# Kernel tuning notes

Measured on AMD Instinct MI355X. Metric: run time of the kernel, lower is better.

The kernel has to match this reference:

```python
import jax, jax.numpy as jnp
import numpy as np


def _ln(x, g, eps=1e-5):
    # channel LayerNorm over dim 1, unbiased=False variance
    mean = jnp.mean(x, axis=1, keepdims=True)
    var = jnp.mean((x - mean) ** 2, axis=1, keepdims=True)
    return (x - mean) * jax.lax.rsqrt(var + eps) * g


def _c11(x, w, b):
    # 1x1 conv: w (O,C), b (O,)
    return jnp.einsum('bchw,oc->bohw', x, w) + b[None, :, None, None]


def _dw(x, w, b):
    # depthwise 3x3 conv, SAME padding; w (C,1,3,3), b (C,)
    C = x.shape[1]
    y = jax.lax.conv_general_dilated(x, w, (1, 1), 'SAME',
                                     feature_group_count=C,
                                     dimension_numbers=('NCHW', 'OIHW', 'NCHW'))
    return y + b[None, :, None, None]


def _forward(F_i, F_w, g1, g2, qw1, qb1, kw1, kb1, vw1, vb1,
             qw2, qb2, kw2, kb2, vw2, vb2,
             qdw1, qdb1, kdw1, kdb1, vdw1, vdb1,
             qdw2, qdb2, kdw2, kdb2, vdw2, vdb2, lw, lb):
    B, C1, H, W = F_i.shape
    C2 = F_w.shape[1]
    HW = H * W
    fi = _ln(F_i, g1)
    fw = _ln(F_w, g2)
    # qkv = 1x1 conv -> depthwise conv; then RAW C-order reshape (torch .view)
    Qi = _dw(_c11(fi, qw1, qb1), qdw1, qdb1).reshape(B, HW, C1)
    Ki = _dw(_c11(fi, kw1, kb1), kdw1, kdb1).reshape(B, HW, C1)
    Vi = _dw(_c11(fi, vw1, vb1), vdw1, vdb1).reshape(B, C1, HW)
    Qw = _dw(_c11(fw, qw2, qb2), qdw2, qdb2).reshape(B, HW, C2)
    Kw = _dw(_c11(fw, kw2, kb2), kdw2, kdb2).reshape(B, HW, C2)
    Vw = _dw(_c11(fw, vw2, vb2), vdw2, vdb2).reshape(B, C2, HW)
    # channel cross-attention: (B,C1,HW)@(B,HW,C2) -> (B,C1,C2)
    a1 = jax.nn.softmax(jnp.einsum('bnc,bnd->bcd', Qi, Kw), axis=-1)
    a2 = jax.nn.softmax(jnp.einsum('bnc,bnd->bcd', Qw, Ki), axis=-1)
    Aw = jnp.einsum('bcd,bdn->bcn', a1, Vw).reshape(B, H, W, C2).transpose(0, 3, 1, 2)
    Ai = jnp.einsum('bcd,bdn->bcn', a2, Vi).reshape(B, H, W, C1).transpose(0, 3, 1, 2)
    cat = jnp.concatenate([Aw, Ai], axis=1)  # (B, C2+C1, H, W)
    Ct = cat.shape[1]
    flat = cat.reshape(B, Ct, HW).transpose(0, 2, 1).reshape(-1, Ct)  # (B*HW, Ct)
    out = flat @ lw.T + lb  # (B*HW, Cout)
    Cout = lb.shape[0]
    # faithful replication of torch's view/permute/view tail
    out = out.reshape(B, Cout, H, W).transpose(0, 2, 3, 1).reshape(B, Cout, H, W)
    return out + F_i + F_w


def setup_inputs() -> dict:
    key = jax.random.key(0)
    ks = jax.random.split(key, 20)
    B, C, H, W = 8, 128, 128, 128
    d = {}
    d['F_i'] = jax.random.normal(ks[0], (B, C, H, W), jnp.float32)
    d['F_w'] = jax.random.normal(ks[1], (B, C, H, W), jnp.float32)
    d['g1'] = jnp.ones((1, C, 1, 1), jnp.float32)
    d['g2'] = jnp.ones((1, C, 1, 1), jnp.float32)
    s = 1.0 / np.sqrt(C)
    i = 2
    for n in ['qw1', 'kw1', 'vw1', 'qw2', 'kw2', 'vw2']:
        d[n] = jax.random.normal(ks[i], (C, C), jnp.float32) * s
        i += 1
    for n in ['qb1', 'kb1', 'vb1', 'qb2', 'kb2', 'vb2']:
        d[n] = jnp.zeros((C,), jnp.float32)
    sd = 1.0 / 3.0
    for n in ['qdw1', 'kdw1', 'vdw1', 'qdw2', 'kdw2', 'vdw2']:
        d[n] = jax.random.normal(ks[i], (C, 1, 3, 3), jnp.float32) * sd
        i += 1
    for n in ['qdb1', 'kdb1', 'vdb1', 'qdb2', 'kdb2', 'vdb2']:
        d[n] = jnp.zeros((C,), jnp.float32)
    d['lw'] = jax.random.normal(ks[i], (C, 2 * C), jnp.float32) * (1.0 / np.sqrt(2 * C))
    d['lb'] = jnp.zeros((C,), jnp.float32)
    return d


def reference(F_i, F_w, g1, g2, qw1, qb1, kw1, kb1, vw1, vb1,
              qw2, qb2, kw2, kb2, vw2, vb2,
              qdw1, qdb1, kdw1, kdb1, vdw1, vdb1,
              qdw2, qdb2, kdw2, kdb2, vdw2, vdb2, lw, lb):
    return _forward(F_i, F_w, g1, g2, qw1, qb1, kw1, kb1, vw1, vb1,
                    qw2, qb2, kw2, kb2, vw2, vb2,
                    qdw1, qdb1, kdw1, kdb1, vdw1, vdb1,
                    qdw2, qdb2, kdw2, kdb2, vdw2, vdb2, lw, lb)
```

## Files before the change

### kernel.cpp

```cpp
#include <hip/hip_runtime.h>
#include <cstddef>
#include <cstring>

#define HW 16384
#define CC 128
#define NB 8
#define GB 4

typedef short bf16x8_t __attribute__((ext_vector_type(8)));
typedef float floatx4 __attribute__((ext_vector_type(4)));

__device__ inline unsigned short f2bf(float f) {
  unsigned u; __builtin_memcpy(&u, &f, 4);
  u += 0x7fffu + ((u >> 16) & 1u);
  return (unsigned short)(u >> 16);
}
__device__ inline float bf2f(unsigned short s) {
  unsigned u = ((unsigned)s) << 16; float f; __builtin_memcpy(&f, &u, 4);
  return f;
}

__global__ __launch_bounds__(256) void k_ln_stats(const float* __restrict__ x,
                                                  float* __restrict__ mean,
                                                  float* __restrict__ rstd) {
  int idx = blockIdx.x * 256 + threadIdx.x;
  int b = idx >> 14;
  int p = idx & (HW - 1);
  const float* xp = x + ((size_t)b << 21) + p;
  float s = 0.f, ss = 0.f;
  for (int c = 0; c < CC; ++c) {
    float v = xp[(size_t)c << 14];
    s += v;
    ss += v * v;
  }
  float m = s * (1.0f / CC);
  float var = ss * (1.0f / CC) - m * m;
  mean[idx] = m;
  rstd[idx] = rsqrtf(var + 1e-5f);
}

__global__ __launch_bounds__(256) void k_conv1x1_mfma(
    const float* __restrict__ X, const float* __restrict__ W,
    const float* __restrict__ bias, const float* __restrict__ g,
    const float* __restrict__ mean, const float* __restrict__ rstd,
    float* __restrict__ Y, int b0) {
  __shared__ __align__(16) float raw[32][132];
  __shared__ __align__(16) short Ah[128][40];
  __shared__ __align__(16) short Al[128][40];
  __shared__ __align__(16) short Bh[128][40];
  __shared__ __align__(16) short Bl[128][40];
  const int bl = blockIdx.y;
  const int b = b0 + bl;
  const int p0 = blockIdx.x * 128;
  const int t = threadIdx.x;
  const int lane = t & 63, wv = t >> 6;
  const int quad = lane >> 4, l15 = lane & 15;
  const int wr = wv >> 1, wc = wv & 1;

  const int s1c = t >> 3, s1p = (t & 7) * 16;
  const int sao = t >> 1, sas = (t & 1) * 16;
  const int s2p = t & 127, s2o = t >> 7;
  const float mu = mean[b * HW + p0 + s2p];
  const float rs = rstd[b * HW + p0 + s2p];

  const float* Xb = X + ((size_t)b << 21);
  floatx4 acc[4][4];
#pragma unroll
  for (int i = 0; i < 4; ++i)
#pragma unroll
    for (int j = 0; j < 4; ++j) acc[i][j] = (floatx4){0.f, 0.f, 0.f, 0.f};

  for (int k0 = 0; k0 < 128; k0 += 32) {
    {
      const float* xp = Xb + ((size_t)(k0 + s1c) << 14) + p0 + s1p;
#pragma unroll
      for (int u = 0; u < 4; ++u)
        *reinterpret_cast<float4*>(&raw[s1c][s1p + 4 * u]) =
            *reinterpret_cast<const float4*>(xp + 4 * u);
    }
    {
      const float* wp = W + sao * 128 + k0 + sas;
      const float* gp = g + k0 + sas;
      short th[16], tl[16];
#pragma unroll
      for (int j = 0; j < 16; ++j) {
        float v = wp[j] * gp[j];
        unsigned short h = f2bf(v);
        th[j] = (short)h;
        tl[j] = (short)f2bf(v - bf2f(h));
      }
#pragma unroll
      for (int j = 0; j < 2; ++j) {
        *reinterpret_cast<bf16x8_t*>(&Ah[sao][sas + 8 * j]) =
            *reinterpret_cast<bf16x8_t*>(&th[8 * j]);
        *reinterpret_cast<bf16x8_t*>(&Al[sao][sas + 8 * j]) =
            *reinterpret_cast<bf16x8_t*>(&tl[8 * j]);
      }
    }
    __syncthreads();
#pragma unroll
    for (int item = 0; item < 2; ++item) {
      const int oct = s2o + 2 * item;
      short th[8], tl[8];
#pragma unroll
      for (int jj = 0; jj < 8; ++jj) {
        float v = (raw[oct * 8 + jj][s2p] - mu) * rs;
        unsigned short h = f2bf(v);
        th[jj] = (short)h;
        tl[jj] = (short)f2bf(v - bf2f(h));
      }
      *reinterpret_cast<bf16x8_t*>(&Bh[s2p][oct * 8]) =
          *reinterpret_cast<bf16x8_t*>(&th[0]);
      *reinterpret_cast<bf16x8_t*>(&Bl[s2p][oct * 8]) =
          *reinterpret_cast<bf16x8_t*>(&tl[0]);
    }
    __syncthreads();
    bf16x8_t afh[4], afl[4], bfh[4], bfl[4];
#pragma unroll
    for (int i = 0; i < 4; ++i) {
      const int m = wr * 64 + i * 16 + l15;
      afh[i] = *reinterpret_cast<const bf16x8_t*>(&Ah[m][quad * 8]);
      afl[i] = *reinterpret_cast<const bf16x8_t*>(&Al[m][quad * 8]);
    }
#pragma unroll
    for (int j = 0; j < 4; ++j) {
      const int p = wc * 64 + j * 16 + l15;
      bfh[j] = *reinterpret_cast<const bf16x8_t*>(&Bh[p][quad * 8]);
      bfl[j] = *reinterpret_cast<const bf16x8_t*>(&Bl[p][quad * 8]);
    }
#pragma unroll
    for (int i = 0; i < 4; ++i)
#pragma unroll
      for (int j = 0; j < 4; ++j) {
        acc[i][j] = __builtin_amdgcn_mfma_f32_16x16x32_bf16(afh[i], bfh[j], acc[i][j], 0, 0, 0);
        acc[i][j] = __builtin_amdgcn_mfma_f32_16x16x32_bf16(afh[i], bfl[j], acc[i][j], 0, 0, 0);
        acc[i][j] = __builtin_amdgcn_mfma_f32_16x16x32_bf16(afl[i], bfh[j], acc[i][j], 0, 0, 0);
      }
    __syncthreads();
  }
  float* Yb = Y + ((size_t)bl << 21);
#pragma unroll
  for (int i = 0; i < 4; ++i) {
#pragma unroll
    for (int j = 0; j < 4; ++j) {
#pragma unroll
      for (int r = 0; r < 4; ++r) {
        const int o = wr * 64 + i * 16 + quad * 4 + r;
        const int p = p0 + wc * 64 + j * 16 + l15;
        Yb[((size_t)o << 14) + p] = acc[i][j][r] + bias[o];
      }
    }
  }
}

__global__ __launch_bounds__(256) void k_score_mfma(
    const float* __restrict__ Yq, const float* __restrict__ Yk,
    const float* __restrict__ qdw, const float* __restrict__ qdb,
    const float* __restrict__ kdw, const float* __restrict__ kdb,
    float* __restrict__ P) {
  __shared__ __align__(16) float raw[32][132];
  __shared__ __align__(16) short Ah[128][40];
  __shared__ __align__(16) short Al[128][40];
  __shared__ __align__(16) short Bh[128][40];
  __shared__ __align__(16) short Bl[128][40];
  const int ch = blockIdx.x;
  const int bl = blockIdx.y;
  const int t = threadIdx.x;
  const int lane = t & 63, wv = t >> 6;
  const int quad = lane >> 4, l15 = lane & 15;
  const int wr = wv >> 1, wc = wv & 1;
  const int h_loc = t >> 3;
  const int w0 = (t & 7) * 16;
  const int s2w = t & 127, s2o = t >> 7;
  const int cc = ch;
  const float* Yqb = Yq + ((size_t)bl << 21) + ((size_t)cc << 14);
  const float* Ykb = Yk + ((size_t)bl << 21) + ((size_t)cc << 14);
  const float* qwt = qdw + cc * 9;
  const float* kwt = kdw + cc * 9;
  const float qbv = qdb[cc], kbv = kdb[cc];

  floatx4 acc[4][4];
#pragma unroll
  for (int i = 0; i < 4; ++i)
#pragma unroll
    for (int j = 0; j < 4; ++j) acc[i][j] = (floatx4){0.f, 0.f, 0.f, 0.f};

  for (int k0 = 0; k0 < 128; k0 += 32) {
    const int h = k0 + h_loc;
#pragma unroll
    for (int side = 0; side < 2; ++side) {
      const float* Yc = side ? Ykb : Yqb;
      const float* wt = side ? kwt : qwt;
      const float bias = side ? kbv : qbv;
      float a[16];
#pragma unroll
      for (int j = 0; j < 16; ++j) a[j] = bias;
#pragma unroll
      for (int dy = 0; dy < 3; ++dy) {
        const int hh = h + dy - 1;
        if (hh < 0 || hh > 127) continue;
        const float* rp = Yc + (hh << 7) + w0;
        float4 f0 = *reinterpret_cast<const float4*>(rp);
        float4 f1 = *reinterpret_cast<const float4*>(rp + 4);
        float4 f2 = *reinterpret_cast<const float4*>(rp + 8);
        float4 f3 = *reinterpret_cast<const float4*>(rp + 12);
        float s[18];
        s[1] = f0.x;  s[2] = f0.y;  s[3] = f0.z;  s[4] = f0.w;
        s[5] = f1.x;  s[6] = f1.y;  s[7] = f1.z;  s[8] = f1.w;
        s[9] = f2.x;  s[10] = f2.y; s[11] = f2.z; s[12] = f2.w;
        s[13] = f3.x; s[14] = f3.y; s[15] = f3.z; s[16] = f3.w;
        s[0] = (w0 > 0) ? rp[-1] : 0.f;
        s[17] = (w0 < 112) ? rp[16] : 0.f;
        const float wa = wt[dy * 3 + 0], wb = wt[dy * 3 + 1], wc2 = wt[dy * 3 + 2];
#pragma unroll
        for (int j = 0; j < 16; ++j)
          a[j] = fmaf(s[j], wa, fmaf(s[j + 1], wb, fmaf(s[j + 2], wc2, a[j])));
      }
#pragma unroll
      for (int u = 0; u < 4; ++u)
        *reinterpret_cast<float4*>(&raw[h_loc][w0 + 4 * u]) =
            (float4){a[4 * u], a[4 * u + 1], a[4 * u + 2], a[4 * u + 3]};
      __syncthreads();
      short* dh = side ? &Bh[0][0] : &Ah[0][0];
      short* dl = side ? &Bl[0][0] : &Al[0][0];
#pragma unroll
      for (int item = 0; item < 2; ++item) {
        const int oct = s2o + 2 * item;
        short th[8], tl[8];
#pragma unroll
        for (int jj = 0; jj < 8; ++jj) {
          float v = raw[oct * 8 + jj][s2w];
          unsigned short hb = f2bf(v);
          th[jj] = (short)hb;
          tl[jj] = (short)f2bf(v - bf2f(hb));
        }
        *reinterpret_cast<bf16x8_t*>(&dh[s2w * 40 + oct * 8]) =
            *reinterpret_cast<bf16x8_t*>(&th[0]);
        *reinterpret_cast<bf16x8_t*>(&dl[s2w * 40 + oct * 8]) =
            *reinterpret_cast<bf16x8_t*>(&tl[0]);
      }
      __syncthreads();
    }
    bf16x8_t afh[4], afl[4], bfh[4], bfl[4];
#pragma unroll
    for (int i = 0; i < 4; ++i) {
      const int m = wr * 64 + i * 16 + l15;
      afh[i] = *reinterpret_cast<const bf16x8_t*>(&Ah[m][quad * 8]);
      afl[i] = *reinterpret_cast<const bf16x8_t*>(&Al[m][quad * 8]);
    }
#pragma unroll
    for (int j = 0; j < 4; ++j) {
      const int n = wc * 64 + j * 16 + l15;
      bfh[j] = *reinterpret_cast<const bf16x8_t*>(&Bh[n][quad * 8]);
      bfl[j] = *reinterpret_cast<const bf16x8_t*>(&Bl[n][quad * 8]);
    }
#pragma unroll
    for (int i = 0; i < 4; ++i)
#pragma unroll
      for (int j = 0; j < 4; ++j) {
        acc[i][j] = __builtin_amdgcn_mfma_f32_16x16x32_bf16(afh[i], bfh[j], acc[i][j], 0, 0, 0);
        acc[i][j] = __builtin_amdgcn_mfma_f32_16x16x32_bf16(afh[i], bfl[j], acc[i][j], 0, 0, 0);
        acc[i][j] = __builtin_amdgcn_mfma_f32_16x16x32_bf16(afl[i], bfh[j], acc[i][j], 0, 0, 0);
      }
  }
  float* Pp = P + ((size_t)(ch * GB + bl) << 14);
#pragma unroll
  for (int i = 0; i < 4; ++i) {
#pragma unroll
    for (int j = 0; j < 4; ++j) {
#pragma unroll
      for (int r = 0; r < 4; ++r) {
        const int c = wr * 64 + i * 16 + quad * 4 + r;
        const int d = wc * 64 + j * 16 + l15;
        Pp[c * 128 + d] = acc[i][j][r];
      }
    }
  }
}

__global__ __launch_bounds__(256) void k_score_reduce(const float* __restrict__ P,
                                                      float* __restrict__ S) {
  int idx = blockIdx.x * 256 + threadIdx.x;
  int bl = idx >> 14;
  int rem = idx & 16383;
  float s = 0.f;
  for (int c = 0; c < 128; ++c) s += P[((size_t)(c * GB + bl) << 14) + rem];
  S[idx] = s;
}

__global__ __launch_bounds__(128) void k_softmax(float* __restrict__ S) {
  __shared__ float red[128];
  const int row = blockIdx.x;
  const int t = threadIdx.x;
  float v = S[row * 128 + t];
  red[t] = v;
  __syncthreads();
  for (int s = 64; s > 0; s >>= 1) {
    if (t < s) red[t] = fmaxf(red[t], red[t + s]);
    __syncthreads();
  }
  float mx = red[0];
  __syncthreads();
  float e = expf(v - mx);
  red[t] = e;
  __syncthreads();
  for (int s = 64; s > 0; s >>= 1) {
    if (t < s) red[t] += red[t + s];
    __syncthreads();
  }
  S[row * 128 + t] = e / red[0];
}

__global__ __launch_bounds__(256) void k_dw_t(const float* __restrict__ Y,
                                              const float* __restrict__ Kw,
                                              const float* __restrict__ db,
                                              unsigned short* __restrict__ Vt) {
  __shared__ unsigned short T[128][33];
  const int h = blockIdx.x;
  const int c0 = blockIdx.y * 32;
  const int bl = blockIdx.z;
  const int t = threadIdx.x;
  const int cl = t >> 3;
  const int w0 = (t & 7) * 16;
  const int c = c0 + cl;
  const float* Yc = Y + ((size_t)bl << 21) + ((size_t)c << 14);
  const float* wt = Kw + c * 9;
  float a[16];
#pragma unroll
  for (int j = 0; j < 16; ++j) a[j] = db[c];
#pragma unroll
  for (int dy = 0; dy < 3; ++dy) {
    const int hh = h + dy - 1;
    if (hh < 0 || hh > 127) continue;
    const float* rp = Yc + (hh << 7) + w0;
    float4 f0 = *reinterpret_cast<const float4*>(rp);
    float4 f1 = *reinterpret_cast<const float4*>(rp + 4);
    float4 f2 = *reinterpret_cast<const float4*>(rp + 8);
    float4 f3 = *reinterpret_cast<const float4*>(rp + 12);
    float s[18];
    s[1] = f0.x;  s[2] = f0.y;  s[3] = f0.z;  s[4] = f0.w;
    s[5] = f1.x;  s[6] = f1.y;  s[7] = f1.z;  s[8] = f1.w;
    s[9] = f2.x;  s[10] = f2.y; s[11] = f2.z; s[12] = f2.w;
    s[13] = f3.x; s[14] = f3.y; s[15] = f3.z; s[16] = f3.w;
    s[0] = (w0 > 0) ? rp[-1] : 0.f;
    s[17] = (w0 < 112) ? rp[16] : 0.f;
    const float wa = wt[dy * 3 + 0], wb = wt[dy * 3 + 1], wc2 = wt[dy * 3 + 2];
#pragma unroll
    for (int j = 0; j < 16; ++j)
      a[j] = fmaf(s[j], wa, fmaf(s[j + 1], wb, fmaf(s[j + 2], wc2, a[j])));
  }
#pragma unroll
  for (int j = 0; j < 16; ++j) T[w0 + j][cl] = f2bf(a[j]);
  __syncthreads();
  const int w = t >> 1, half = t & 1;
  unsigned short tmp[16];
#pragma unroll
  for (int j = 0; j < 16; ++j) tmp[j] = T[w][half * 16 + j];
  uint4 v0, v1;
  unsigned* vp0 = reinterpret_cast<unsigned*>(&v0);
  unsigned* vp1 = reinterpret_cast<unsigned*>(&v1);
#pragma unroll
  for (int j = 0; j < 4; ++j) {
    vp0[j] = (unsigned)tmp[2 * j] | ((unsigned)tmp[2 * j + 1] << 16);
    vp1[j] = (unsigned)tmp[8 + 2 * j] | ((unsigned)tmp[8 + 2 * j + 1] << 16);
  }
  unsigned short* dst = Vt + ((size_t)bl << 21) + ((size_t)((h << 7) + w) << 7)
                        + c0 + half * 16;
  *reinterpret_cast<uint4*>(dst) = v0;
  *reinterpret_cast<uint4*>(dst + 8) = v1;
}

__global__ __launch_bounds__(256) void k_av_mfma(
    const float* __restrict__ S, const unsigned short* __restrict__ Vt,
    unsigned short* __restrict__ O) {
  __shared__ __align__(16) short As[128][136];
  const int bl = blockIdx.y;
  const int p0 = blockIdx.x * 128;
  const int t = threadIdx.x;
  const int lane = t & 63, wv = t >> 6;
  const int quad = lane >> 4, l15 = lane & 15;
  const int wr = wv >> 1, wc = wv & 1;
  {
    const float* Ab = S + ((size_t)bl << 14);
    const int r = t >> 1, hf = (t & 1) * 64;
    const float* src = Ab + r * 128 + hf;
    short tmp[64];
#pragma unroll
    for (int j = 0; j < 64; ++j) tmp[j] = (short)f2bf(src[j]);
#pragma unroll
    for (int j = 0; j < 8; ++j)
      *reinterpret_cast<bf16x8_t*>(&As[r][hf + j * 8]) =
          *reinterpret_cast<bf16x8_t*>(&tmp[j * 8]);
  }
  __syncthreads();
  floatx4 acc[4][4];
#pragma unroll
  for (int i = 0; i < 4; ++i)
#pragma unroll
    for (int j = 0; j < 4; ++j) acc[i][j] = (floatx4){0.f, 0.f, 0.f, 0.f};
  const unsigned short* Vb = Vt + ((size_t)bl << 21);
#pragma unroll
  for (int d0 = 0; d0 < 128; d0 += 32) {
    bf16x8_t af[4], bf[4];
#pragma unroll
    for (int i = 0; i < 4; ++i) {
      const int m = wr * 64 + i * 16 + l15;
      af[i] = *reinterpret_cast<const bf16x8_t*>(&As[m][d0 + quad * 8]);
    }
#pragma unroll
    for (int j = 0; j < 4; ++j) {
      const int p = p0 + wc * 64 + j * 16 + l15;
      bf[j] = *reinterpret_cast<const bf16x8_t*>(Vb + ((size_t)p << 7) + d0 + quad * 8);
    }
#pragma unroll
    for (int i = 0; i < 4; ++i)
#pragma unroll
      for (int j = 0; j < 4; ++j)
        acc[i][j] = __builtin_amdgcn_mfma_f32_16x16x32_bf16(af[i], bf[j], acc[i][j], 0, 0, 0);
  }
  unsigned short* Ob = O + ((size_t)bl << 21);
#pragma unroll
  for (int i = 0; i < 4; ++i) {
#pragma unroll
    for (int j = 0; j < 4; ++j) {
#pragma unroll
      for (int r = 0; r < 4; ++r) {
        const int c = wr * 64 + i * 16 + quad * 4 + r;
        const int p = p0 + wc * 64 + j * 16 + l15;
        Ob[((size_t)c << 14) + p] = f2bf(acc[i][j][r]);
      }
    }
  }
}

__global__ __launch_bounds__(256) void k_final2_mfma(
    const unsigned short* __restrict__ A1, const unsigned short* __restrict__ A2,
    const float* __restrict__ lw, const float* __restrict__ lb,
    const float* __restrict__ Fi, const float* __restrict__ Fw,
    float* __restrict__ out, int b0) {
  __shared__ __align__(16) short As[128][136];
  const int c2 = blockIdx.x;
  const int bl = blockIdx.y;
  const int b = b0 + bl;
  const int t = threadIdx.x;
  const int lane = t & 63, wv = t >> 6;
  const int quad = lane >> 4, l15 = lane & 15;
  const int wr = wv >> 1, wc = wv & 1;
  floatx4 acc[4][4];
#pragma unroll
  for (int i = 0; i < 4; ++i)
#pragma unroll
    for (int j = 0; j < 4; ++j) acc[i][j] = (floatx4){0.f, 0.f, 0.f, 0.f};
#pragma unroll
  for (int phase = 0; phase < 2; ++phase) {
    {
      const int r = t >> 1, hf = (t & 1) * 64;
      const float* src = lw + r * 256 + phase * 128 + hf;
      short tmp[64];
#pragma unroll
      for (int j = 0; j < 64; ++j) tmp[j] = (short)f2bf(src[j]);
#pragma unroll
      for (int j = 0; j < 8; ++j)
        *reinterpret_cast<bf16x8_t*>(&As[r][hf + j * 8]) =
            *reinterpret_cast<bf16x8_t*>(&tmp[j * 8]);
    }
    __syncthreads();
    const unsigned short* Ub = (phase ? A2 : A1) + ((size_t)bl << 21) + c2 * 128;
#pragma unroll
    for (int d0 = 0; d0 < 128; d0 += 32) {
      bf16x8_t af[4], bf[4];
#pragma unroll
      for (int i = 0; i < 4; ++i) {
        const int m = wr * 64 + i * 16 + l15;
        af[i] = *reinterpret_cast<const bf16x8_t*>(&As[m][d0 + quad * 8]);
      }
#pragma unroll
      for (int j = 0; j < 4; ++j) {
        const int n = wc * 64 + j * 16 + l15;
        bf[j] = *reinterpret_cast<const bf16x8_t*>(Ub + ((size_t)n << 14) + d0 + quad * 8);
      }
#pragma unroll
      for (int i = 0; i < 4; ++i)
#pragma unroll
        for (int j = 0; j < 4; ++j)
          acc[i][j] = __builtin_amdgcn_mfma_f32_16x16x32_bf16(af[i], bf[j], acc[i][j], 0, 0, 0);
    }
    __syncthreads();
  }
  const size_t obase = ((size_t)b << 21) + ((size_t)c2 << 14);
#pragma unroll
  for (int i = 0; i < 4; ++i) {
#pragma unroll
    for (int j = 0; j < 4; ++j) {
#pragma unroll
      for (int r = 0; r < 4; ++r) {
        const int h2 = wr * 64 + i * 16 + quad * 4 + r;
        const int w2 = wc * 64 + j * 16 + l15;
        const size_t a = obase + ((size_t)h2 << 7) + w2;
        out[a] = acc[i][j][r] + lb[h2] + Fi[a] + Fw[a];
      }
    }
  }
}

extern "C" void kernel_launch(void* const* d_in, const int* in_sizes, int n_in,
                              void* d_out, int out_size, void* d_ws, size_t ws_size,
                              hipStream_t stream) {
  const float* F_i  = (const float*)d_in[0];
  const float* F_w  = (const float*)d_in[1];
  const float* g1   = (const float*)d_in[2];
  const float* g2   = (const float*)d_in[3];
  const float* qw1  = (const float*)d_in[4];
  const float* kw1  = (const float*)d_in[5];
  const float* vw1  = (const float*)d_in[6];
  const float* qw2  = (const float*)d_in[7];
  const float* kw2  = (const float*)d_in[8];
  const float* vw2  = (const float*)d_in[9];
  const float* qb1  = (const float*)d_in[10];
  const float* kb1  = (const float*)d_in[11];
  const float* vb1  = (const float*)d_in[12];
  const float* qb2  = (const float*)d_in[13];
  const float* kb2  = (const float*)d_in[14];
  const float* vb2  = (const float*)d_in[15];
  const float* qdw1 = (const float*)d_in[16];
  const float* kdw1 = (const float*)d_in[17];
  const float* vdw1 = (const float*)d_in[18];
  const float* qdw2 = (const float*)d_in[19];
  const float* kdw2 = (const float*)d_in[20];
  const float* vdw2 = (const float*)d_in[21];
  const float* qdb1 = (const float*)d_in[22];
  const float* kdb1 = (const float*)d_in[23];
  const float* vdb1 = (const float*)d_in[24];
  const float* qdb2 = (const float*)d_in[25];
  const float* kdb2 = (const float*)d_in[26];
  const float* vdb2 = (const float*)d_in[27];
  const float* lw   = (const float*)d_in[28];
  const float* lb   = (const float*)d_in[29];
  float* out = (float*)d_out;

  char* w = (char*)d_ws;
  const size_t NTOT = (size_t)NB * HW;
  float* meanI = (float*)w; w += NTOT * 4;
  float* rstdI = (float*)w; w += NTOT * 4;
  float* meanW = (float*)w; w += NTOT * 4;
  float* rstdW = (float*)w; w += NTOT * 4;
  float* S     = (float*)w; w += (size_t)GB * HW * 4;
  float* P     = (float*)w; w += (size_t)128 * GB * HW * 4;
  float* Yq    = (float*)w; w += ((size_t)GB << 21) * 4;
  char*  Ykreg = w;         w += ((size_t)GB << 21) * 4;
  float* Yk    = (float*)Ykreg;
  unsigned short* Vt = (unsigned short*)Ykreg;
  unsigned short* A2 = (unsigned short*)(Ykreg + ((size_t)GB << 21) * 2);
  unsigned short* A1 = (unsigned short*)w; w += ((size_t)GB << 21) * 2;

  dim3 blk(256);
  k_ln_stats<<<dim3(512), blk, 0, stream>>>(F_i, meanI, rstdI);
  k_ln_stats<<<dim3(512), blk, 0, stream>>>(F_w, meanW, rstdW);

  for (int b0 = 0; b0 < NB; b0 += GB) {
    k_conv1x1_mfma<<<dim3(128, GB), blk, 0, stream>>>(F_i, qw1, qb1, g1, meanI, rstdI, Yq, b0);
    k_conv1x1_mfma<<<dim3(128, GB), blk, 0, stream>>>(F_w, kw2, kb2, g2, meanW, rstdW, Yk, b0);
    k_score_mfma<<<dim3(128, GB), blk, 0, stream>>>(Yq, Yk, qdw1, qdb1, kdw2, kdb2, P);
    k_score_reduce<<<dim3(GB * HW / 256), blk, 0, stream>>>(P, S);
    k_softmax<<<dim3(GB * 128), dim3(128), 0, stream>>>(S);
    k_conv1x1_mfma<<<dim3(128, GB), blk, 0, stream>>>(F_w, vw2, vb2, g2, meanW, rstdW, Yq, b0);
    k_dw_t<<<dim3(128, 4, GB), blk, 0, stream>>>(Yq, vdw2, vdb2, Vt);
    k_av_mfma<<<dim3(128, GB), blk, 0, stream>>>(S, Vt, A1);

    k_conv1x1_mfma<<<dim3(128, GB), blk, 0, stream>>>(F_w, qw2, qb2, g2, meanW, rstdW, Yq, b0);
    k_conv1x1_mfma<<<dim3(128, GB), blk, 0, stream>>>(F_i, kw1, kb1, g1, meanI, rstdI, Yk, b0);
    k_score_mfma<<<dim3(128, GB), blk, 0, stream>>>(Yq, Yk, qdw2, qdb2, kdw1, kdb1, P);
    k_score_reduce<<<dim3(GB * HW / 256), blk, 0, stream>>>(P, S);
    k_softmax<<<dim3(GB * 128), dim3(128), 0, stream>>>(S);
    k_conv1x1_mfma<<<dim3(128, GB), blk, 0, stream>>>(F_i, vw1, vb1, g1, meanI, rstdI, Yq, b0);
    k_dw_t<<<dim3(128, 4, GB), blk, 0, stream>>>(Yq, vdw1, vdb1, Vt);
    k_av_mfma<<<dim3(128, GB), blk, 0, stream>>>(S, Vt, A2);

    k_final2_mfma<<<dim3(128, GB), blk, 0, stream>>>(A1, A2, lw, lb, F_i, F_w, out, b0);
  }
}
```

Before: 843.2 us.

## Fuse K/V projections and replace per-channel score partials with atomic accumulation

Adds a kernel that computes the K and V 1x1 projections together, so the normalized input tile is loaded and converted once per pass instead of twice. The score kernel no longer writes one partial matrix per channel block into a large buffer; it atomically adds into 8 partial slices. Reduction of those slices is fused into the softmax kernel, which removes the separate reduce kernel and a large write/read of partial sums. This adds a zeroing launch and atomic contention, and the workspace is re-laid out so the partial buffer aliases the A2 region.

```diff
diff --git a/kernel.cpp b/kernel.cpp
--- a/kernel.cpp
+++ b/kernel.cpp
@@ -153,11 +153,164 @@
   }
 }
 
+__global__ __launch_bounds__(256) void k_convKV_mfma(
+    const float* __restrict__ X,
+    const float* __restrict__ Wk, const float* __restrict__ kb,
+    const float* __restrict__ Wv, const float* __restrict__ vb,
+    const float* __restrict__ g,
+    const float* __restrict__ mean, const float* __restrict__ rstd,
+    float* __restrict__ Yk, float* __restrict__ Yv, int b0) {
+  __shared__ __align__(16) float raw[32][68];
+  __shared__ __align__(16) short Kh[128][40];
+  __shared__ __align__(16) short Kl[128][40];
+  __shared__ __align__(16) short Vh[128][40];
+  __shared__ __align__(16) short Vl[128][40];
+  __shared__ __align__(16) short Bh[64][40];
+  __shared__ __align__(16) short Bl[64][40];
+  const int bl = blockIdx.y;
+  const int b = b0 + bl;
+  const int p0 = blockIdx.x * 64;
+  const int t = threadIdx.x;
+  const int lane = t & 63, wv = t >> 6;
+  const int quad = lane >> 4, l15 = lane & 15;
+  const int wr = wv >> 1, wc = wv & 1;
+
+  const int s1c = t >> 3, s1p = (t & 7) * 8;
+  const int sao = t >> 1, sas = (t & 1) * 16;
+  const int s2p = t & 63, s2o = t >> 6;
+  const float mu = mean[b * HW + p0 + s2p];
+  const float rs = rstd[b * HW + p0 + s2p];
+
+  const float* Xb = X + ((size_t)b << 21);
+  floatx4 accK[4][2], accV[4][2];
+#pragma unroll
+  for (int i = 0; i < 4; ++i)
+#pragma unroll
+    for (int j = 0; j < 2; ++j) {
+      accK[i][j] = (floatx4){0.f, 0.f, 0.f, 0.f};
+      accV[i][j] = (floatx4){0.f, 0.f, 0.f, 0.f};
+    }
+
+  for (int k0 = 0; k0 < 128; k0 += 32) {
+    {
+      const float* xp = Xb + ((size_t)(k0 + s1c) << 14) + p0 + s1p;
+      *reinterpret_cast<float4*>(&raw[s1c][s1p]) =
+          *reinterpret_cast<const float4*>(xp);
+      *reinterpret_cast<float4*>(&raw[s1c][s1p + 4]) =
+          *reinterpret_cast<const float4*>(xp + 4);
+    }
+    {
+      const float* gp = g + k0 + sas;
+      const float* wkp = Wk + sao * 128 + k0 + sas;
+      const float* wvp = Wv + sao * 128 + k0 + sas;
+      short th[16], tl[16];
+#pragma unroll
+      for (int j = 0; j < 16; ++j) {
+        float v = wkp[j] * gp[j];
+        unsigned short h = f2bf(v);
+        th[j] = (short)h;
+        tl[j] = (short)f2bf(v - bf2f(h));
+      }
+#pragma unroll
+      for (int j = 0; j < 2; ++j) {
+        *reinterpret_cast<bf16x8_t*>(&Kh[sao][sas + 8 * j]) =
+            *reinterpret_cast<bf16x8_t*>(&th[8 * j]);
+        *reinterpret_cast<bf16x8_t*>(&Kl[sao][sas + 8 * j]) =
+            *reinterpret_cast<bf16x8_t*>(&tl[8 * j]);
+      }
+#pragma unroll
+      for (int j = 0; j < 16; ++j) {
+        float v = wvp[j] * gp[j];
+        unsigned short h = f2bf(v);
+        th[j] = (short)h;
+        tl[j] = (short)f2bf(v - bf2f(h));
+      }
+#pragma unroll
+      for (int j = 0; j < 2; ++j) {
+        *reinterpret_cast<bf16x8_t*>(&Vh[sao][sas + 8 * j]) =
+            *reinterpret_cast<bf16x8_t*>(&th[8 * j]);
+        *reinterpret_cast<bf16x8_t*>(&Vl[sao][sas + 8 * j]) =
+            *reinterpret_cast<bf16x8_t*>(&tl[8 * j]);
+      }
+    }
+    __syncthreads();
+    {
+      short th[8], tl[8];
+#pragma unroll
+      for (int jj = 0; jj < 8; ++jj) {
+        float v = (raw[s2o * 8 + jj][s2p] - mu) * rs;
+        unsigned short h = f2bf(v);
+        th[jj] = (short)h;
+        tl[jj] = (short)f2bf(v - bf2f(h));
+      }
+      *reinterpret_cast<bf16x8_t*>(&Bh[s2p][s2o * 8]) =
+          *reinterpret_cast<bf16x8_t*>(&th[0]);
+      *reinterpret_cast<bf16x8_t*>(&Bl[s2p][s2o * 8]) =
+          *reinterpret_cast<bf16x8_t*>(&tl[0]);
+    }
+    __syncthreads();
+    bf16x8_t bfh[2], bfl[2];
+#pragma unroll
+    for (int j = 0; j < 2; ++j) {
+      const int p = wc * 32 + j * 16 + l15;
+      bfh[j] = *reinterpret_cast<const bf16x8_t*>(&Bh[p][quad * 8]);
+      bfl[j] = *reinterpret_cast<const bf16x8_t*>(&Bl[p][quad * 8]);
+    }
+    {
+      bf16x8_t ah[4], al[4];
+#pragma unroll
+      for (int i = 0; i < 4; ++i) {
+        const int m = wr * 64 + i * 16 + l15;
+        ah[i] = *reinterpret_cast<const bf16x8_t*>(&Kh[m][quad * 8]);
+        al[i] = *reinterpret_cast<const bf16x8_t*>(&Kl[m][quad * 8]);
+      }
+#pragma unroll
+      for (int i = 0; i < 4; ++i)
+#pragma unroll
+        for (int j = 0; j < 2; ++j) {
+          accK[i][j] = __builtin_amdgcn_mfma_f32_16x16x32_bf16(ah[i], bfh[j], accK[i][j], 0, 0, 0);
+          accK[i][j] = __builtin_amdgcn_mfma_f32_16x16x32_bf16(ah[i], bfl[j], accK[i][j], 0, 0, 0);
+          accK[i][j] = __builtin_amdgcn_mfma_f32_16x16x32_bf16(al[i], bfh[j], accK[i][j], 0, 0, 0);
+        }
+#pragma unroll
+      for (int i = 0; i < 4; ++i) {
+        const int m = wr * 64 + i * 16 + l15;
+        ah[i] = *reinterpret_cast<const bf16x8_t*>(&Vh[m][quad * 8]);
+        al[i] = *reinterpret_cast<const bf16x8_t*>(&Vl[m][quad * 8]);
+      }
+#pragma unroll
+      for (int i = 0; i < 4; ++i)
+#pragma unroll
+        for (int j = 0; j < 2; ++j) {
+          accV[i][j] = __builtin_amdgcn_mfma_f32_16x16x32_bf16(ah[i], bfh[j], accV[i][j], 0, 0, 0);
+          accV[i][j] = __builtin_amdgcn_mfma_f32_16x16x32_bf16(ah[i], bfl[j], accV[i][j], 0, 0, 0);
+          accV[i][j] = __builtin_amdgcn_mfma_f32_16x16x32_bf16(al[i], bfh[j], accV[i][j], 0, 0, 0);
+        }
+    }
+    __syncthreads();
+  }
+  float* Ykb = Yk + ((size_t)bl << 21);
+  float* Yvb = Yv + ((size_t)bl << 21);
+#pragma unroll
+  for (int i = 0; i < 4; ++i) {
+#pragma unroll
+    for (int j = 0; j < 2; ++j) {
+#pragma unroll
+      for (int r = 0; r < 4; ++r) {
+        const int o = wr * 64 + i * 16 + quad * 4 + r;
+        const int p = p0 + wc * 32 + j * 16 + l15;
+        Ykb[((size_t)o << 14) + p] = accK[i][j][r] + kb[o];
+        Yvb[((size_t)o << 14) + p] = accV[i][j][r] + vb[o];
+      }
+    }
+  }
+}
+
 __global__ __launch_bounds__(256) void k_score_mfma(
     const float* __restrict__ Yq, const float* __restrict__ Yk,
     const float* __restrict__ qdw, const float* __restrict__ qdb,
     const float* __restrict__ kdw, const float* __restrict__ kdb,
-    float* __restrict__ P) {
+    float* __restrict__ P8) {
   __shared__ __align__(16) float raw[32][132];
   __shared__ __align__(16) short Ah[128][40];
   __shared__ __align__(16) short Al[128][40];
@@ -263,7 +416,7 @@
         acc[i][j] = __builtin_amdgcn_mfma_f32_16x16x32_bf16(afl[i], bfh[j], acc[i][j], 0, 0, 0);
       }
   }
-  float* Pp = P + ((size_t)(ch * GB + bl) << 14);
+  float* Pp = P8 + ((size_t)((ch & 7) * GB + bl) << 14);
 #pragma unroll
   for (int i = 0; i < 4; ++i) {
 #pragma unroll
@@ -272,27 +425,26 @@
       for (int r = 0; r < 4; ++r) {
         const int c = wr * 64 + i * 16 + quad * 4 + r;
         const int d = wc * 64 + j * 16 + l15;
-        Pp[c * 128 + d] = acc[i][j][r];
-      }
-    }
-  }
-}
-
-__global__ __launch_bounds__(256) void k_score_reduce(const float* __restrict__ P,
-                                                      float* __restrict__ S) {
-  int idx = blockIdx.x * 256 + threadIdx.x;
-  int bl = idx >> 14;
-  int rem = idx & 16383;
-  float s = 0.f;
-  for (int c = 0; c < 128; ++c) s += P[((size_t)(c * GB + bl) << 14) + rem];
-  S[idx] = s;
-}
-
-__global__ __launch_bounds__(128) void k_softmax(float* __restrict__ S) {
+        (void)__hip_atomic_fetch_add(&Pp[c * 128 + d], acc[i][j][r],
+                                     __ATOMIC_RELAXED, __HIP_MEMORY_SCOPE_AGENT);
+      }
+    }
+  }
+}
+
+__global__ __launch_bounds__(256) void k_zero(float4* __restrict__ p) {
+  p[blockIdx.x * 256 + threadIdx.x] = (float4){0.f, 0.f, 0.f, 0.f};
+}
+
+__global__ __launch_bounds__(128) void k_reduce8_softmax(
+    const float* __restrict__ P8, float* __restrict__ S) {
   __shared__ float red[128];
   const int row = blockIdx.x;
   const int t = threadIdx.x;
-  float v = S[row * 128 + t];
+  const size_t base = ((size_t)row << 7) + t;
+  float v = 0.f;
+#pragma unroll
+  for (int k = 0; k < 8; ++k) v += P8[(((size_t)(k * GB)) << 14) + base];
   red[t] = v;
   __syncthreads();
   for (int s = 64; s > 0; s >>= 1) {
@@ -308,7 +460,7 @@
     if (t < s) red[t] += red[t + s];
     __syncthreads();
   }
-  S[row * 128 + t] = e / red[0];
+  S[base] = e / red[0];
 }
 
 __global__ __launch_bounds__(256) void k_dw_t(const float* __restrict__ Y,
@@ -545,35 +697,35 @@
   float* meanW = (float*)w; w += NTOT * 4;
   float* rstdW = (float*)w; w += NTOT * 4;
   float* S     = (float*)w; w += (size_t)GB * HW * 4;
-  float* P     = (float*)w; w += (size_t)128 * GB * HW * 4;
-  float* Yq    = (float*)w; w += ((size_t)GB << 21) * 4;
-  char*  Ykreg = w;         w += ((size_t)GB << 21) * 4;
-  float* Yk    = (float*)Ykreg;
-  unsigned short* Vt = (unsigned short*)Ykreg;
-  unsigned short* A2 = (unsigned short*)(Ykreg + ((size_t)GB << 21) * 2);
   unsigned short* A1 = (unsigned short*)w; w += ((size_t)GB << 21) * 2;
+  unsigned short* A2 = (unsigned short*)w;
+  float* P8 = (float*)A2;
+  w += ((size_t)GB << 21) * 2;
+  float* Yk  = (float*)w; w += ((size_t)GB << 21) * 4;
+  float* Yqv = (float*)w; w += ((size_t)GB << 21) * 4;
+  unsigned short* Vt = (unsigned short*)w; w += ((size_t)GB << 21) * 2;
 
   dim3 blk(256);
   k_ln_stats<<<dim3(512), blk, 0, stream>>>(F_i, meanI, rstdI);
   k_ln_stats<<<dim3(512), blk, 0, stream>>>(F_w, meanW, rstdW);
 
   for (int b0 = 0; b0 < NB; b0 += GB) {
-    k_conv1x1_mfma<<<dim3(128, GB), blk, 0, stream>>>(F_i, qw1, qb1, g1, meanI, rstdI, Yq, b0);
-    k_conv1x1_mfma<<<dim3(128, GB), blk, 0, stream>>>(F_w, kw2, kb2, g2, meanW, rstdW, Yk, b0);
-    k_score_mfma<<<dim3(128, GB), blk, 0, stream>>>(Yq, Yk, qdw1, qdb1, kdw2, kdb2, P);
-    k_score_reduce<<<dim3(GB * HW / 256), blk, 0, stream>>>(P, S);
-    k_softmax<<<dim3(GB * 128), dim3(128), 0, stream>>>(S);
-    k_conv1x1_mfma<<<dim3(128, GB), blk, 0, stream>>>(F_w, vw2, vb2, g2, meanW, rstdW, Yq, b0);
-    k_dw_t<<<dim3(128, 4, GB), blk, 0, stream>>>(Yq, vdw2, vdb2, Vt);
+    k_convKV_mfma<<<dim3(256, GB), blk, 0, stream>>>(F_w, kw2, kb2, vw2, vb2,
+                                                     g2, meanW, rstdW, Yk, Yqv, b0);
+    k_dw_t<<<dim3(128, 4, GB), blk, 0, stream>>>(Yqv, vdw2, vdb2, Vt);
+    k_conv1x1_mfma<<<dim3(128, GB), blk, 0, stream>>>(F_i, qw1, qb1, g1, meanI, rstdI, Yqv, b0);
+    k_zero<<<dim3(512), blk, 0, stream>>>((float4*)P8);
+    k_score_mfma<<<dim3(128, GB), blk, 0, stream>>>(Yqv, Yk, qdw1, qdb1, kdw2, kdb2, P8);
+    k_reduce8_softmax<<<dim3(GB * 128), dim3(128), 0, stream>>>(P8, S);
     k_av_mfma<<<dim3(128, GB), blk, 0, stream>>>(S, Vt, A1);
 
-    k_conv1x1_mfma<<<dim3(128, GB), blk, 0, stream>>>(F_w, qw2, qb2, g2, meanW, rstdW, Yq, b0);
-    k_conv1x1_mfma<<<dim3(128, GB), blk, 0, stream>>>(F_i, kw1, kb1, g1, meanI, rstdI, Yk, b0);
-    k_score_mfma<<<dim3(128, GB), blk, 0, stream>>>(Yq, Yk, qdw2, qdb2, kdw1, kdb1, P);
-    k_score_reduce<<<dim3(GB * HW / 256), blk, 0, stream>>>(P, S);
-    k_softmax<<<dim3(GB * 128), dim3(128), 0, stream>>>(S);
-    k_conv1x1_mfma<<<dim3(128, GB), blk, 0, stream>>>(F_i, vw1, vb1, g1, meanI, rstdI, Yq, b0);
-    k_dw_t<<<dim3(128, 4, GB), blk, 0, stream>>>(Yq, vdw1, vdb1, Vt);
+    k_convKV_mfma<<<dim3(256, GB), blk, 0, stream>>>(F_i, kw1, kb1, vw1, vb1,
+                                                     g1, meanI, rstdI, Yk, Yqv, b0);
+    k_dw_t<<<dim3(128, 4, GB), blk, 0, stream>>>(Yqv, vdw1, vdb1, Vt);
+    k_conv1x1_mfma<<<dim3(128, GB), blk, 0, stream>>>(F_w, qw2, qb2, g2, meanW, rstdW, Yqv, b0);
+    k_zero<<<dim3(512), blk, 0, stream>>>((float4*)P8);
+    k_score_mfma<<<dim3(128, GB), blk, 0, stream>>>(Yqv, Yk, qdw2, qdb2, kdw1, kdb1, P8);
+    k_reduce8_softmax<<<dim3(GB * 128), dim3(128), 0, stream>>>(P8, S);
     k_av_mfma<<<dim3(128, GB), blk, 0, stream>>>(S, Vt, A2);
 
     k_final2_mfma<<<dim3(128, GB), blk, 0, stream>>>(A1, A2, lw, lb, F_i, F_w, out, b0);
```

Measured after the change: 927.6 us. 1.1x slower.

## Precompute split-bf16 weights once and fuse score reduce with softmax

Applied to the files above, without the earlier changes.

Adds a prep kernel that converts the six gamma-scaled 1x1 conv weights into hi/lo bf16 pairs and converts the final linear weight to bf16 once per call. The conv, AV and final kernels then read these fragments straight from global memory and no longer convert per block through shared memory. The partial-score reduction and softmax become one kernel that writes bf16 probabilities. This removes redundant conversion work, a launch and some syncs, at the cost of uncoalesced global fragment loads that depend on cache hits.

```diff
diff --git a/kernel.cpp b/kernel.cpp
--- a/kernel.cpp
+++ b/kernel.cpp
@@ -18,6 +18,39 @@
 __device__ inline float bf2f(unsigned short s) {
   unsigned u = ((unsigned)s) << 16; float f; __builtin_memcpy(&f, &u, 4);
   return f;
+}
+
+__global__ __launch_bounds__(256) void k_prep_w(
+    const float* __restrict__ qw1, const float* __restrict__ kw1,
+    const float* __restrict__ vw1, const float* __restrict__ qw2,
+    const float* __restrict__ kw2, const float* __restrict__ vw2,
+    const float* __restrict__ g1, const float* __restrict__ g2,
+    const float* __restrict__ lw,
+    unsigned short* __restrict__ Wsplit, unsigned short* __restrict__ lwbf) {
+  const int t = threadIdx.x;
+  const int m = blockIdx.y;
+  if (m < 6) {
+    const float* W = (m == 0) ? qw1 : (m == 1) ? kw1 : (m == 2) ? vw1
+                   : (m == 3) ? qw2 : (m == 4) ? kw2 : vw2;
+    const float* g = (m < 3) ? g1 : g2;
+    const int idx = blockIdx.x * 256 + t;
+    const int o = idx >> 4;
+    const int c0 = (idx & 15) * 8;
+    unsigned short* hi = Wsplit + m * 32768 + o * 128 + c0;
+    unsigned short* lo = hi + 16384;
+#pragma unroll
+    for (int j = 0; j < 8; ++j) {
+      float v = W[o * 128 + c0 + j] * g[c0 + j];
+      unsigned short h = f2bf(v);
+      hi[j] = h;
+      lo[j] = f2bf(v - bf2f(h));
+    }
+  } else {
+    const int idx = blockIdx.x * 256 + t;
+#pragma unroll
+    for (int j = 0; j < 16; ++j)
+      lwbf[idx * 16 + j] = f2bf(lw[idx * 16 + j]);
+  }
 }
 
 __global__ __launch_bounds__(256) void k_ln_stats(const float* __restrict__ x,
@@ -40,13 +73,12 @@
 }
 
 __global__ __launch_bounds__(256) void k_conv1x1_mfma(
-    const float* __restrict__ X, const float* __restrict__ W,
-    const float* __restrict__ bias, const float* __restrict__ g,
+    const float* __restrict__ X,
+    const unsigned short* __restrict__ Whi, const unsigned short* __restrict__ Wlo,
+    const float* __restrict__ bias,
     const float* __restrict__ mean, const float* __restrict__ rstd,
     float* __restrict__ Y, int b0) {
   __shared__ __align__(16) float raw[32][132];
-  __shared__ __align__(16) short Ah[128][40];
-  __shared__ __align__(16) short Al[128][40];
   __shared__ __align__(16) short Bh[128][40];
   __shared__ __align__(16) short Bl[128][40];
   const int bl = blockIdx.y;
@@ -58,7 +90,6 @@
   const int wr = wv >> 1, wc = wv & 1;
 
   const int s1c = t >> 3, s1p = (t & 7) * 16;
-  const int sao = t >> 1, sas = (t & 1) * 16;
   const int s2p = t & 127, s2o = t >> 7;
   const float mu = mean[b * HW + p0 + s2p];
   const float rs = rstd[b * HW + p0 + s2p];
@@ -77,25 +108,6 @@
       for (int u = 0; u < 4; ++u)
         *reinterpret_cast<float4*>(&raw[s1c][s1p + 4 * u]) =
             *reinterpret_cast<const float4*>(xp + 4 * u);
-    }
-    {
-      const float* wp = W + sao * 128 + k0 + sas;
-      const float* gp = g + k0 + sas;
-      short th[16], tl[16];
-#pragma unroll
-      for (int j = 0; j < 16; ++j) {
-        float v = wp[j] * gp[j];
-        unsigned short h = f2bf(v);
-        th[j] = (short)h;
-        tl[j] = (short)f2bf(v - bf2f(h));
-      }
-#pragma unroll
-      for (int j = 0; j < 2; ++j) {
-        *reinterpret_cast<bf16x8_t*>(&Ah[sao][sas + 8 * j]) =
-            *reinterpret_cast<bf16x8_t*>(&th[8 * j]);
-        *reinterpret_cast<bf16x8_t*>(&Al[sao][sas + 8 * j]) =
-            *reinterpret_cast<bf16x8_t*>(&tl[8 * j]);
-      }
     }
     __syncthreads();
 #pragma unroll
@@ -119,8 +131,8 @@
 #pragma unroll
     for (int i = 0; i < 4; ++i) {
       const int m = wr * 64 + i * 16 + l15;
-      afh[i] = *reinterpret_cast<const bf16x8_t*>(&Ah[m][quad * 8]);
-      afl[i] = *reinterpret_cast<const bf16x8_t*>(&Al[m][quad * 8]);
+      afh[i] = *reinterpret_cast<const bf16x8_t*>(Whi + m * 128 + k0 + quad * 8);
+      afl[i] = *reinterpret_cast<const bf16x8_t*>(Wlo + m * 128 + k0 + quad * 8);
     }
 #pragma unroll
     for (int j = 0; j < 4; ++j) {
@@ -278,21 +290,16 @@
   }
 }
 
-__global__ __launch_bounds__(256) void k_score_reduce(const float* __restrict__ P,
-                                                      float* __restrict__ S) {
-  int idx = blockIdx.x * 256 + threadIdx.x;
-  int bl = idx >> 14;
-  int rem = idx & 16383;
-  float s = 0.f;
-  for (int c = 0; c < 128; ++c) s += P[((size_t)(c * GB + bl) << 14) + rem];
-  S[idx] = s;
-}
-
-__global__ __launch_bounds__(128) void k_softmax(float* __restrict__ S) {
+__global__ __launch_bounds__(128) void k_reduce_softmax(
+    const float* __restrict__ P, unsigned short* __restrict__ Sbf) {
   __shared__ float red[128];
   const int row = blockIdx.x;
-  const int t = threadIdx.x;
-  float v = S[row * 128 + t];
+  const int bl = row >> 7, c = row & 127;
+  const int t = threadIdx.x;
+  const size_t rem = ((size_t)c << 7) + t;
+  float v = 0.f;
+  for (int ch = 0; ch < 128; ++ch)
+    v += P[((size_t)(ch * GB + bl) << 14) + rem];
   red[t] = v;
   __syncthreads();
   for (int s = 64; s > 0; s >>= 1) {
@@ -308,7 +315,7 @@
     if (t < s) red[t] += red[t + s];
     __syncthreads();
   }
-  S[row * 128 + t] = e / red[0];
+  Sbf[((size_t)bl << 14) + rem] = f2bf(e / red[0]);
 }
 
 __global__ __launch_bounds__(256) void k_dw_t(const float* __restrict__ Y,
@@ -371,28 +378,15 @@
 }
 
 __global__ __launch_bounds__(256) void k_av_mfma(
-    const float* __restrict__ S, const unsigned short* __restrict__ Vt,
+    const unsigned short* __restrict__ Sbf, const unsigned short* __restrict__ Vt,
     unsigned short* __restrict__ O) {
-  __shared__ __align__(16) short As[128][136];
   const int bl = blockIdx.y;
   const int p0 = blockIdx.x * 128;
   const int t = threadIdx.x;
   const int lane = t & 63, wv = t >> 6;
   const int quad = lane >> 4, l15 = lane & 15;
   const int wr = wv >> 1, wc = wv & 1;
-  {
-    const float* Ab = S + ((size_t)bl << 14);
-    const int r = t >> 1, hf = (t & 1) * 64;
-    const float* src = Ab + r * 128 + hf;
-    short tmp[64];
-#pragma unroll
-    for (int j = 0; j < 64; ++j) tmp[j] = (short)f2bf(src[j]);
-#pragma unroll
-    for (int j = 0; j < 8; ++j)
-      *reinterpret_cast<bf16x8_t*>(&As[r][hf + j * 8]) =
-          *reinterpret_cast<bf16x8_t*>(&tmp[j * 8]);
-  }
-  __syncthreads();
+  const unsigned short* Sb = Sbf + ((size_t)bl << 14);
   floatx4 acc[4][4];
 #pragma unroll
   for (int i = 0; i < 4; ++i)
@@ -405,7 +399,7 @@
 #pragma unroll
     for (int i = 0; i < 4; ++i) {
       const int m = wr * 64 + i * 16 + l15;
-      af[i] = *reinterpret_cast<const bf16x8_t*>(&As[m][d0 + quad * 8]);
+      af[i] = *reinterpret_cast<const bf16x8_t*>(Sb + m * 128 + d0 + quad * 8);
     }
 #pragma unroll
     for (int j = 0; j < 4; ++j) {
@@ -435,10 +429,9 @@
 
 __global__ __launch_bounds__(256) void k_final2_mfma(
     const unsigned short* __restrict__ A1, const unsigned short* __restrict__ A2,
-    const float* __restrict__ lw, const float* __restrict__ lb,
+    const unsigned short* __restrict__ lwbf, const float* __restrict__ lb,
     const float* __restrict__ Fi, const float* __restrict__ Fw,
     float* __restrict__ out, int b0) {
-  __shared__ __align__(16) short As[128][136];
   const int c2 = blockIdx.x;
   const int bl = blockIdx.y;
   const int b = b0 + bl;
@@ -453,18 +446,6 @@
     for (int j = 0; j < 4; ++j) acc[i][j] = (floatx4){0.f, 0.f, 0.f, 0.f};
 #pragma unroll
   for (int phase = 0; phase < 2; ++phase) {
-    {
-      const int r = t >> 1, hf = (t & 1) * 64;
-      const float* src = lw + r * 256 + phase * 128 + hf;
-      short tmp[64];
-#pragma unroll
-      for (int j = 0; j < 64; ++j) tmp[j] = (short)f2bf(src[j]);
-#pragma unroll
-      for (int j = 0; j < 8; ++j)
-        *reinterpret_cast<bf16x8_t*>(&As[r][hf + j * 8]) =
-            *reinterpret_cast<bf16x8_t*>(&tmp[j * 8]);
-    }
-    __syncthreads();
     const unsigned short* Ub = (phase ? A2 : A1) + ((size_t)bl << 21) + c2 * 128;
 #pragma unroll
     for (int d0 = 0; d0 < 128; d0 += 32) {
@@ -472,7 +453,8 @@
 #pragma unroll
       for (int i = 0; i < 4; ++i) {
         const int m = wr * 64 + i * 16 + l15;
-        af[i] = *reinterpret_cast<const bf16x8_t*>(&As[m][d0 + quad * 8]);
+        af[i] = *reinterpret_cast<const bf16x8_t*>(
+            lwbf + m * 256 + phase * 128 + d0 + quad * 8);
       }
 #pragma unroll
       for (int j = 0; j < 4; ++j) {
@@ -485,7 +467,6 @@
         for (int j = 0; j < 4; ++j)
           acc[i][j] = __builtin_amdgcn_mfma_f32_16x16x32_bf16(af[i], bf[j], acc[i][j], 0, 0, 0);
     }
-    __syncthreads();
   }
   const size_t obase = ((size_t)b << 21) + ((size_t)c2 << 14);
 #pragma unroll
@@ -544,7 +525,9 @@
   float* rstdI = (float*)w; w += NTOT * 4;
   float* meanW = (float*)w; w += NTOT * 4;
   float* rstdW = (float*)w; w += NTOT * 4;
-  float* S     = (float*)w; w += (size_t)GB * HW * 4;
+  unsigned short* Sbf = (unsigned short*)w; w += (size_t)GB * HW * 2;
+  unsigned short* Wsplit = (unsigned short*)w; w += 6 * 32768 * 2;
+  unsigned short* lwbf = (unsigned short*)w; w += 32768 * 2;
   float* P     = (float*)w; w += (size_t)128 * GB * HW * 4;
   float* Yq    = (float*)w; w += ((size_t)GB << 21) * 4;
   char*  Ykreg = w;         w += ((size_t)GB << 21) * 4;
@@ -553,29 +536,36 @@
   unsigned short* A2 = (unsigned short*)(Ykreg + ((size_t)GB << 21) * 2);
   unsigned short* A1 = (unsigned short*)w; w += ((size_t)GB << 21) * 2;
 
+  const unsigned short* Wh0 = Wsplit + 0 * 32768;
+  const unsigned short* Wh1 = Wsplit + 1 * 32768;
+  const unsigned short* Wh2 = Wsplit + 2 * 32768;
+  const unsigned short* Wh3 = Wsplit + 3 * 32768;
+  const unsigned short* Wh4 = Wsplit + 4 * 32768;
+  const unsigned short* Wh5 = Wsplit + 5 * 32768;
+
   dim3 blk(256);
+  k_prep_w<<<dim3(8, 7), blk, 0, stream>>>(qw1, kw1, vw1, qw2, kw2, vw2,
+                                           g1, g2, lw, Wsplit, lwbf);
   k_ln_stats<<<dim3(512), blk, 0, stream>>>(F_i, meanI, rstdI);
   k_ln_stats<<<dim3(512), blk, 0, stream>>>(F_w, meanW, rstdW);
 
   for (int b0 = 0; b0 < NB; b0 += GB) {
-    k_conv1x1_mfma<<<dim3(128, GB), blk, 0, stream>>>(F_i, qw1, qb1, g1, meanI, rstdI, Yq, b0);
-    k_conv1x1_mfma<<<dim3(128, GB), blk, 0, stream>>>(F_w, kw2, kb2, g2, meanW, rstdW, Yk, b0);
+    k_conv1x1_mfma<<<dim3(128, GB), blk, 0, stream>>>(F_i, Wh0, Wh0 + 16384, qb1, meanI, rstdI, Yq, b0);
+    k_conv1x1_mfma<<<dim3(128, GB), blk, 0, stream>>>(F_w, Wh4, Wh4 + 16384, kb2, meanW, rstdW, Yk, b0);
     k_score_mfma<<<dim3(128, GB), blk, 0, stream>>>(Yq, Yk, qdw1, qdb1, kdw2, kdb2, P);
-    k_score_reduce<<<dim3(GB * HW / 256), blk, 0, stream>>>(P, S);
-    k_softmax<<<dim3(GB * 128), dim3(128), 0, stream>>>(S);
-    k_conv1x1_mfma<<<dim3(128, GB), blk, 0, stream>>>(F_w, vw2, vb2, g2, meanW, rstdW, Yq, b0);
+    k_reduce_softmax<<<dim3(GB * 128), dim3(128), 0, stream>>>(P, Sbf);
+    k_conv1x1_mfma<<<dim3(128, GB), blk, 0, stream>>>(F_w, Wh5, Wh5 + 16384, vb2, meanW, rstdW, Yq, b0);
     k_dw_t<<<dim3(128, 4, GB), blk, 0, stream>>>(Yq, vdw2, vdb2, Vt);
-    k_av_mfma<<<dim3(128, GB), blk, 0, stream>>>(S, Vt, A1);
-
-    k_conv1x1_mfma<<<dim3(128, GB), blk, 0, stream>>>(F_w, qw2, qb2, g2, meanW, rstdW, Yq, b0);
-    k_conv1x1_mfma<<<dim3(128, GB), blk, 0, stream>>>(F_i, kw1, kb1, g1, meanI, rstdI, Yk, b0);
+    k_av_mfma<<<dim3(128, GB), blk, 0, stream>>>(Sbf, Vt, A1);
+
+    k_conv1x1_mfma<<<dim3(128, GB), blk, 0, stream>>>(F_w, Wh3, Wh3 + 16384, qb2, meanW, rstdW, Yq, b0);
+    k_conv1x1_mfma<<<dim3(128, GB), blk, 0, stream>>>(F_i, Wh1, Wh1 + 16384, kb1, meanI, rstdI, Yk, b0);
     k_score_mfma<<<dim3(128, GB), blk, 0, stream>>>(Yq, Yk, qdw2, qdb2, kdw1, kdb1, P);
-    k_score_reduce<<<dim3(GB * HW / 256), blk, 0, stream>>>(P, S);
-    k_softmax<<<dim3(GB * 128), dim3(128), 0, stream>>>(S);
-    k_conv1x1_mfma<<<dim3(128, GB), blk, 0, stream>>>(F_i, vw1, vb1, g1, meanI, rstdI, Yq, b0);
+    k_reduce_softmax<<<dim3(GB * 128), dim3(128), 0, stream>>>(P, Sbf);
+    k_conv1x1_mfma<<<dim3(128, GB), blk, 0, stream>>>(F_i, Wh2, Wh2 + 16384, vb1, meanI, rstdI, Yq, b0);
     k_dw_t<<<dim3(128, 4, GB), blk, 0, stream>>>(Yq, vdw1, vdb1, Vt);
-    k_av_mfma<<<dim3(128, GB), blk, 0, stream>>>(S, Vt, A2);
-
-    k_final2_mfma<<<dim3(128, GB), blk, 0, stream>>>(A1, A2, lw, lb, F_i, F_w, out, b0);
-  }
-}
+    k_av_mfma<<<dim3(128, GB), blk, 0, stream>>>(Sbf, Vt, A2);
+
+    k_final2_mfma<<<dim3(128, GB), blk, 0, stream>>>(A1, A2, lwbf, lb, F_i, F_w, out, b0);
+  }
+}
```

After: 808.5 us. -4.1%, faster.
